# Performance work log

Hardware: AMD Instinct MI355X
Metric: run time of the kernel (lower is better)

## Reference

```python
import jax, jax.numpy as jnp
import numpy as np

B, H, W, C = 32, 56, 56, 192
NUM_HEADS = 6
WS = 7
SHIFT = 3
HIDDEN = 4 * C


def _relative_position_index(ws):
    coords = np.stack(np.meshgrid(np.arange(ws), np.arange(ws), indexing="ij"))  # 2,ws,ws
    coords = coords.reshape(2, -1)
    rel = coords[:, :, None] - coords[:, None, :]  # 2,N,N
    rel = rel.transpose(1, 2, 0)
    rel[:, :, 0] += ws - 1
    rel[:, :, 1] += ws - 1
    rel[:, :, 0] *= 2 * ws - 1
    return rel.sum(-1)  # N,N in [0, (2ws-1)^2)


def setup_inputs() -> dict:
    key = jax.random.key(0)
    ks = jax.random.split(key, 16)
    s = 0.02
    inp = {
        "x": jax.random.normal(ks[0], (B, H, W, C), jnp.float32),
        "norm1_g": jnp.ones((C,), jnp.float32),
        "norm1_b": jnp.zeros((C,), jnp.float32),
        "qkv_w": jax.random.normal(ks[1], (3 * C, C), jnp.float32) * s,
        "qkv_b": jnp.zeros((3 * C,), jnp.float32),
        "proj_w": jax.random.normal(ks[2], (C, C), jnp.float32) * s,
        "proj_b": jnp.zeros((C,), jnp.float32),
        "rel_bias_table": jax.random.normal(ks[3], ((2 * WS - 1) ** 2, NUM_HEADS), jnp.float32) * s,
        "norm2_g": jnp.ones((C,), jnp.float32),
        "norm2_b": jnp.zeros((C,), jnp.float32),
        "fc1_w": jax.random.normal(ks[4], (HIDDEN, C), jnp.float32) * s,
        "fc1_b": jnp.zeros((HIDDEN,), jnp.float32),
        "fc2_w": jax.random.normal(ks[5], (C, HIDDEN), jnp.float32) * s,
        "fc2_b": jnp.zeros((C,), jnp.float32),
        "rel_index": jnp.asarray(_relative_position_index(WS), jnp.int32),  # (49,49)
    }
    return inp


def _layernorm(x, g, b, eps=1e-5):
    mu = x.mean(-1, keepdims=True)
    var = ((x - mu) ** 2).mean(-1, keepdims=True)
    return (x - mu) * jax.lax.rsqrt(var + eps) * g + b


def _window_partition(x, ws):
    b, h, w, c = x.shape
    x = x.reshape(b, h // ws, ws, w // ws, ws, c)
    return x.transpose(0, 1, 3, 2, 4, 5).reshape(-1, ws * ws, c)


def _window_reverse(win, ws, b, h, w):
    c = win.shape[-1]
    x = win.reshape(b, h // ws, w // ws, ws, ws, c)
    return x.transpose(0, 1, 3, 2, 4, 5).reshape(b, h, w, c)


def reference(x, norm1_g, norm1_b, qkv_w, qkv_b, proj_w, proj_b, rel_bias_table,
              norm2_g, norm2_b, fc1_w, fc1_b, fc2_w, fc2_b, rel_index):
    shortcut = x
    xn = _layernorm(x, norm1_g, norm1_b)
    xs = jnp.roll(xn, (-SHIFT, -SHIFT), axis=(1, 2))
    win = _window_partition(xs, WS)  # (nW*B, 49, C)
    nw, n, c = win.shape
    hd = c // NUM_HEADS
    qkv = win @ qkv_w.T + qkv_b  # (nw, n, 3C)
    qkv = qkv.reshape(nw, n, 3, NUM_HEADS, hd).transpose(2, 0, 3, 1, 4)
    q, k, v = qkv[0], qkv[1], qkv[2]  # (nw, heads, n, hd)
    q = q * (hd ** -0.5)
    attn = jnp.einsum("whnd,whmd->whnm", q, k)
    bias = rel_bias_table[rel_index.reshape(-1)].reshape(n, n, NUM_HEADS).transpose(2, 0, 1)
    attn = jax.nn.softmax(attn + bias[None], axis=-1)
    out = jnp.einsum("whnm,whmd->whnd", attn, v)
    out = out.transpose(0, 2, 1, 3).reshape(nw, n, c)
    out = out @ proj_w.T + proj_b
    xs = _window_reverse(out, WS, x.shape[0], x.shape[1], x.shape[2])
    xa = jnp.roll(xs, (SHIFT, SHIFT), axis=(1, 2))
    x = shortcut + xa
    xm = _layernorm(x, norm2_g, norm2_b)
    xm = jax.nn.gelu(xm @ fc1_w.T + fc1_b, approximate=False)
    xm = xm @ fc2_w.T + fc2_b
    return x + xm
```

## Files before the change

### kernel.cpp

```cpp
#include <hip/hip_runtime.h>
#include <hip/hip_bf16.h>

#define CC 192
#define NHEADS 6
#define HDIM 32
#define NTOK 49
#define NWIN 2048
#define MTOK 100352
#define HIDDEN 768

typedef __hip_bfloat16 bf16;
typedef __attribute__((ext_vector_type(8))) short short8;
typedef __attribute__((ext_vector_type(4))) float f32x4;

__global__ __launch_bounds__(256) void k_wconv(
    const float* __restrict__ qw, const float* __restrict__ pw,
    const float* __restrict__ f1, const float* __restrict__ f2,
    bf16* __restrict__ o) {
  int i = blockIdx.x * 256 + threadIdx.x;
  if (i < 110592) o[i] = __float2bfloat16(qw[i]);
  else if (i < 147456) o[i] = __float2bfloat16(pw[i - 110592]);
  else if (i < 294912) o[i] = __float2bfloat16(f1[i - 147456]);
  else if (i < 442368) o[i] = __float2bfloat16(f2[i - 294912]);
}

__global__ __launch_bounds__(256) void k_bias(
    const float* __restrict__ table, const int* __restrict__ ridx,
    float* __restrict__ bias6) {
  int i = blockIdx.x * 256 + threadIdx.x;
  if (i >= 6 * 2401) return;
  int h = i / 2401, e = i - h * 2401;
  bias6[i] = table[ridx[e] * NHEADS + h];
}

template <int MODE, int NT, int KC, int MF>
__global__ __launch_bounds__(256) void k_gemm_areg(
    const void* __restrict__ Ap, const bf16* __restrict__ W,
    const float* __restrict__ bias, void* __restrict__ out0,
    const void* __restrict__ aux, const float* __restrict__ lng,
    const float* __restrict__ lnb) {
  constexpr int K = KC * 192;
  constexpr int N = NT * 64;
  __shared__ bf16 Bs[2][64 * 192];
  const int tid = threadIdx.x;
  const int wave = tid >> 6, lane = tid & 63;
  const int grp = lane >> 4, rA = lane & 15;
  const int cq = grp, cn = rA;
  const int m0 = blockIdx.x * (MF * 64);
  const int mrow = m0 + wave * (MF * 16);

  short8 areg[MF][KC * 6];
  if constexpr (MODE == 1) {
#pragma unroll
    for (int mt = 0; mt < MF; ++mt) {
      const bf16* arow =
          (const bf16*)Ap + (size_t)(mrow + mt * 16 + rA) * K + grp * 8;
#pragma unroll
      for (int kt = 0; kt < KC * 6; ++kt)
        areg[mt][kt] = *(const short8*)(arow + kt * 32);
    }
  } else {
#pragma unroll
    for (int mt = 0; mt < MF; ++mt) {
      int m = mrow + mt * 16 + rA;
      int w = m / 49, n = m - w * 49;
      int b = w >> 6, wrem = w & 63;
      int hi = wrem >> 3, wi = wrem & 7;
      int ii = n / 7, jj = n - ii * 7;
      int hs = hi * 7 + ii + 3; if (hs >= 56) hs -= 56;
      int wsc = wi * 7 + jj + 3; if (wsc >= 56) wsc -= 56;
      const float* rowp =
          (const float*)Ap + (size_t)((b * 56 + hs) * 56 + wsc) * CC;
      f32x4 xv[12];
#pragma unroll
      for (int kt = 0; kt < 6; ++kt) {
        xv[2 * kt]     = *(const f32x4*)(rowp + kt * 32 + grp * 8);
        xv[2 * kt + 1] = *(const f32x4*)(rowp + kt * 32 + grp * 8 + 4);
      }
      float s = 0.0f;
#pragma unroll
      for (int i = 0; i < 12; ++i)
#pragma unroll
        for (int j = 0; j < 4; ++j) s += xv[i][j];
      s += __shfl_xor(s, 16, 64);
      s += __shfl_xor(s, 32, 64);
      float mu = s * (1.0f / 192.0f);
      float q = 0.0f;
#pragma unroll
      for (int i = 0; i < 12; ++i)
#pragma unroll
        for (int j = 0; j < 4; ++j) {
          float d = xv[i][j] - mu;
          q += d * d;
        }
      q += __shfl_xor(q, 16, 64);
      q += __shfl_xor(q, 32, 64);
      float inv = rsqrtf(q * (1.0f / 192.0f) + 1e-5f);
#pragma unroll
      for (int kt = 0; kt < 6; ++kt) {
        short8 t;
#pragma unroll
        for (int j = 0; j < 8; ++j) {
          int col = kt * 32 + grp * 8 + j;
          float xval = xv[2 * kt + (j >> 2)][j & 3];
          float val = (xval - mu) * inv * lng[col] + lnb[col];
          bf16 hb = __float2bfloat16(val);
          t[j] = *reinterpret_cast<short*>(&hb);
        }
        areg[mt][kt] = t;
      }
    }
  }

  int rowoff[MF][4];
  if constexpr (MODE == 1) {
#pragma unroll
    for (int mt = 0; mt < MF; ++mt)
#pragma unroll
      for (int r = 0; r < 4; ++r) {
        int m = mrow + mt * 16 + cq * 4 + r;
        int w = m / 49, rr = m - w * 49;
        int b = w >> 6, wrem = w & 63;
        int hi = wrem >> 3, wi = wrem & 7;
        int ii = rr / 7, jj = rr - ii * 7;
        int hd = hi * 7 + ii + 3; if (hd >= 56) hd -= 56;
        int wd = wi * 7 + jj + 3; if (wd >= 56) wd -= 56;
        rowoff[mt][r] = ((b * 56 + hd) * 56 + wd) * CC;
      }
  }

  auto stage = [&](int buf, int nt, int kc) {
#pragma unroll
    for (int i = 0; i < 6; ++i) {
      int c = i * 256 + tid;
      int row = c / 24;
      int cbl = ((c - row * 24) * 16) ^ ((row & 7) << 4);
      const char* src = (const char*)W +
          (size_t)(nt * 64 + row) * (K * 2) + kc * 384 + cbl;
      __builtin_amdgcn_global_load_lds(
          (const __attribute__((address_space(1))) void*)src,
          (__attribute__((address_space(3))) void*)((char*)&Bs[buf][0] + c * 16),
          16, 0, 0);
    }
  };
  stage(0, 0, 0);

  f32x4 acc[MF][4];
#pragma unroll
  for (int s = 0; s < NT * KC; ++s) {
    const int nt = s / KC, kc = s - nt * KC;
    const int cur = s & 1;
    __syncthreads();
    if (s + 1 < NT * KC) stage(cur ^ 1, (s + 1) / KC, (s + 1) % KC);
    if (kc == 0) {
#pragma unroll
      for (int mt = 0; mt < MF; ++mt)
#pragma unroll
        for (int ntf = 0; ntf < 4; ++ntf)
          acc[mt][ntf] = (f32x4){0.f, 0.f, 0.f, 0.f};
    }
#pragma unroll
    for (int kt = 0; kt < 6; ++kt) {
      short8 b[4];
#pragma unroll
      for (int ntf = 0; ntf < 4; ++ntf) {
        int row = ntf * 16 + rA;
        int phys = row * 384 + ((kt * 64 + grp * 16) ^ ((row & 7) << 4));
        b[ntf] = *(const short8*)((const char*)&Bs[cur][0] + phys);
      }
#pragma unroll
      for (int mt = 0; mt < MF; ++mt)
#pragma unroll
        for (int ntf = 0; ntf < 4; ++ntf)
          acc[mt][ntf] = __builtin_amdgcn_mfma_f32_16x16x32_bf16(
              areg[mt][kc * 6 + kt], b[ntf], acc[mt][ntf], 0, 0, 0);
    }
    if (kc == KC - 1) {
      const int n0t = nt * 64;
      float bi[4];
#pragma unroll
      for (int ntf = 0; ntf < 4; ++ntf) bi[ntf] = bias[n0t + ntf * 16 + cn];
#pragma unroll
      for (int mt = 0; mt < MF; ++mt) {
#pragma unroll
        for (int r = 0; r < 4; ++r) {
          const int m = mrow + mt * 16 + cq * 4 + r;
#pragma unroll
          for (int ntf = 0; ntf < 4; ++ntf) {
            const int n = n0t + ntf * 16 + cn;
            float v = acc[mt][ntf][r] + bi[ntf];
            if constexpr (MODE == 0) {
              ((bf16*)out0)[(size_t)m * N + n] = __float2bfloat16(v);
            } else {
              float res = ((const float*)aux)[(size_t)rowoff[mt][r] + n];
              ((float*)out0)[(size_t)rowoff[mt][r] + n] = v + res;
            }
          }
        }
      }
    }
  }
}

__global__ __launch_bounds__(256) void k_mlp(
    const float* __restrict__ x1, const bf16* __restrict__ W1,
    const bf16* __restrict__ W2, const float* __restrict__ b1,
    const float* __restrict__ b2, float* __restrict__ out,
    const float* __restrict__ lng, const float* __restrict__ lnb) {
  __shared__ bf16 W1s[2][32 * 192];
  __shared__ bf16 W2s[2][192 * 32];
  __shared__ bf16 Hl[4][640];
  const int tid = threadIdx.x;
  const int wave = tid >> 6, lane = tid & 63;
  const int grp = lane >> 4, rA = lane & 15;
  const int mrow = blockIdx.x * 64 + wave * 16;
  char* hb = (char*)&Hl[wave][0];

  short8 areg[6];
  {
    const float* rowp = x1 + (size_t)(mrow + rA) * CC;
    f32x4 xv[12];
#pragma unroll
    for (int kt = 0; kt < 6; ++kt) {
      xv[2 * kt]     = *(const f32x4*)(rowp + kt * 32 + grp * 8);
      xv[2 * kt + 1] = *(const f32x4*)(rowp + kt * 32 + grp * 8 + 4);
    }
    float s = 0.0f;
#pragma unroll
    for (int i = 0; i < 12; ++i)
#pragma unroll
      for (int j = 0; j < 4; ++j) s += xv[i][j];
    s += __shfl_xor(s, 16, 64);
    s += __shfl_xor(s, 32, 64);
    float mu = s * (1.0f / 192.0f);
    float q = 0.0f;
#pragma unroll
    for (int i = 0; i < 12; ++i)
#pragma unroll
      for (int j = 0; j < 4; ++j) {
        float d = xv[i][j] - mu;
        q += d * d;
      }
    q += __shfl_xor(q, 16, 64);
    q += __shfl_xor(q, 32, 64);
    float inv = rsqrtf(q * (1.0f / 192.0f) + 1e-5f);
#pragma unroll
    for (int kt = 0; kt < 6; ++kt) {
      short8 t;
#pragma unroll
      for (int j = 0; j < 8; ++j) {
        int col = kt * 32 + grp * 8 + j;
        float xval = xv[2 * kt + (j >> 2)][j & 3];
        float val = (xval - mu) * inv * lng[col] + lnb[col];
        bf16 hbv = __float2bfloat16(val);
        t[j] = *reinterpret_cast<short*>(&hbv);
      }
      areg[kt] = t;
    }
  }

  auto stage1 = [&](int buf, int c) {
#pragma unroll
    for (int i = 0; i < 3; ++i) {
      int s = i * 256 + tid;
      int row = s / 24, slot = s - row * 24;
      int cbl = (slot * 16) ^ ((row & 7) << 4);
      const char* src = (const char*)W1 + (size_t)(c * 32 + row) * 384 + cbl;
      __builtin_amdgcn_global_load_lds(
          (const __attribute__((address_space(1))) void*)src,
          (__attribute__((address_space(3))) void*)((char*)&W1s[buf][0] + s * 16),
          16, 0, 0);
    }
  };
  auto stage2 = [&](int buf, int c) {
#pragma unroll
    for (int i = 0; i < 3; ++i) {
      int s = i * 256 + tid;
      int row = s >> 2, slot = s & 3;
      int cbl = (slot * 16) ^ (((row >> 1) & 3) << 4);
      const char* src = (const char*)W2 + (size_t)row * 1536 + c * 64 + cbl;
      __builtin_amdgcn_global_load_lds(
          (const __attribute__((address_space(1))) void*)src,
          (__attribute__((address_space(3))) void*)((char*)&W2s[buf][0] + s * 16),
          16, 0, 0);
    }
  };

  f32x4 acc2[12];
#pragma unroll
  for (int nf = 0; nf < 12; ++nf) acc2[nf] = (f32x4){0.f, 0.f, 0.f, 0.f};

  stage1(0, 0);
  stage2(0, 0);
  for (int c = 0; c < 24; ++c) {
    const int cur = c & 1;
    __syncthreads();
    if (c + 1 < 24) { stage1(cur ^ 1, c + 1); stage2(cur ^ 1, c + 1); }
    f32x4 fa[2] = {};
#pragma unroll
    for (int kt = 0; kt < 6; ++kt) {
      short8 bfr[2];
#pragma unroll
      for (int ntf = 0; ntf < 2; ++ntf) {
        int row = ntf * 16 + rA;
        int phys = row * 384 + ((kt * 64 + grp * 16) ^ ((row & 7) << 4));
        bfr[ntf] = *(const short8*)((const char*)&W1s[cur][0] + phys);
      }
#pragma unroll
      for (int ntf = 0; ntf < 2; ++ntf)
        fa[ntf] = __builtin_amdgcn_mfma_f32_16x16x32_bf16(
            areg[kt], bfr[ntf], fa[ntf], 0, 0, 0);
    }
#pragma unroll
    for (int ntf = 0; ntf < 2; ++ntf) {
      float b1v = b1[c * 32 + ntf * 16 + rA];
#pragma unroll
      for (int r = 0; r < 4; ++r) {
        float v = fa[ntf][r] + b1v;
        float u2 = 2.0f * v * (0.7978845608f + 0.0356774081f * v * v);
        float ge = v / (1.0f + __expf(-u2));
        int row = grp * 4 + r;
        *(bf16*)(hb + row * 80 + (ntf * 16 + rA) * 2) = __float2bfloat16(ge);
      }
    }
    short8 a2 = *(const short8*)(hb + rA * 80 + grp * 16);
#pragma unroll
    for (int nf = 0; nf < 12; ++nf) {
      int row = nf * 16 + rA;
      int phys = row * 64 + ((grp * 16) ^ (((row >> 1) & 3) << 4));
      short8 bw = *(const short8*)((const char*)&W2s[cur][0] + phys);
      acc2[nf] = __builtin_amdgcn_mfma_f32_16x16x32_bf16(a2, bw, acc2[nf],
                                                         0, 0, 0);
    }
  }

#pragma unroll
  for (int nf = 0; nf < 12; ++nf) {
    float b2v = b2[nf * 16 + rA];
#pragma unroll
    for (int r = 0; r < 4; ++r) {
      int m = mrow + grp * 4 + r;
      size_t idx = (size_t)m * CC + nf * 16 + rA;
      out[idx] = out[idx] + acc2[nf][r] + b2v;
    }
  }
}

__global__ __launch_bounds__(256) void k_attn_mfma(
    const bf16* __restrict__ qk, const float* __restrict__ bias6,
    bf16* __restrict__ ao) {
  __shared__ bf16 P[4][64 * 72];
  __shared__ bf16 VT[4][32 * 72];
  const int wave = threadIdx.x >> 6, lane = threadIdx.x & 63;
  const int wh = blockIdx.x * 4 + wave;
  const int w = wh / NHEADS, h = wh - w * NHEADS;
  const int rA = lane & 15, kq = (lane >> 4) * 8;
  const int grp = lane >> 4;

  const bf16* qbase = qk + (size_t)(w * 49) * 576 + h * HDIM + kq;

  short8 aq[4], bk[4], vrow[4];
#pragma unroll
  for (int t = 0; t < 4; ++t) {
    const bf16* rp = qbase + (size_t)(t * 16 + rA) * 576;
    aq[t] = *(const short8*)(rp);
    bk[t] = *(const short8*)(rp + 192);
    vrow[t] = *(const short8*)(rp + 384);
  }

  f32x4 S[4][4] = {};
#pragma unroll
  for (int mt = 0; mt < 4; ++mt)
#pragma unroll
    for (int nt = 0; nt < 4; ++nt)
      S[mt][nt] = __builtin_amdgcn_mfma_f32_16x16x32_bf16(
          aq[mt], bk[nt], S[mt][nt], 0, 0, 0);

  bf16* Vw = VT[wave];
  const bf16 zero = __float2bfloat16(0.0f);
#pragma unroll
  for (int t = 0; t < 4; ++t) {
    int tok = t * 16 + rA;
#pragma unroll
    for (int j = 0; j < 8; ++j)
      Vw[(kq + j) * 72 + tok] = (tok < 49) ? ((const bf16*)&vrow[t])[j] : zero;
  }

  const float scale = 0.17677669529663687f;
  const float* bh = bias6 + h * 2401;
  float rs[4][4];
  bf16* Pw = P[wave];
#pragma unroll
  for (int mt = 0; mt < 4; ++mt) {
#pragma unroll
    for (int r = 0; r < 4; ++r) {
      int row = mt * 16 + grp * 4 + r;
      float val[4];
#pragma unroll
      for (int nt = 0; nt < 4; ++nt) {
        int c = nt * 16 + rA;
        float bv = (row < 49 && c < 49) ? bh[row * 49 + c] : 0.0f;
        val[nt] = (c < 49) ? (S[mt][nt][r] * scale + bv) : -1e30f;
      }
      float mx = fmaxf(fmaxf(val[0], val[1]), fmaxf(val[2], val[3]));
      for (int m2 = 1; m2 < 16; m2 <<= 1) mx = fmaxf(mx, __shfl_xor(mx, m2, 64));
      float sum = 0.0f;
#pragma unroll
      for (int nt = 0; nt < 4; ++nt) {
        float e = __expf(val[nt] - mx);
        val[nt] = e;
        sum += e;
      }
      for (int m2 = 1; m2 < 16; m2 <<= 1) sum += __shfl_xor(sum, m2, 64);
      rs[mt][r] = 1.0f / sum;
#pragma unroll
      for (int nt = 0; nt < 4; ++nt)
        Pw[row * 72 + nt * 16 + rA] = __float2bfloat16(val[nt]);
    }
  }
  __syncthreads();

  short8 bv[2][2];
#pragma unroll
  for (int ks = 0; ks < 2; ++ks)
#pragma unroll
    for (int nt = 0; nt < 2; ++nt)
      bv[ks][nt] = *(const short8*)&Vw[(nt * 16 + rA) * 72 + ks * 32 + kq];
  f32x4 O[4][2] = {};
#pragma unroll
  for (int mt = 0; mt < 4; ++mt) {
    short8 ap0 = *(const short8*)&Pw[(mt * 16 + rA) * 72 + kq];
    short8 ap1 = *(const short8*)&Pw[(mt * 16 + rA) * 72 + 32 + kq];
#pragma unroll
    for (int nt = 0; nt < 2; ++nt) {
      O[mt][nt] = __builtin_amdgcn_mfma_f32_16x16x32_bf16(ap0, bv[0][nt],
                                                          O[mt][nt], 0, 0, 0);
      O[mt][nt] = __builtin_amdgcn_mfma_f32_16x16x32_bf16(ap1, bv[1][nt],
                                                          O[mt][nt], 0, 0, 0);
    }
  }
#pragma unroll
  for (int mt = 0; mt < 4; ++mt) {
#pragma unroll
    for (int r = 0; r < 4; ++r) {
      int m = mt * 16 + grp * 4 + r;
      if (m < 49) {
        bf16* orow = ao + (size_t)(w * 49 + m) * CC + h * HDIM;
#pragma unroll
        for (int nt = 0; nt < 2; ++nt)
          orow[nt * 16 + rA] = __float2bfloat16(O[mt][nt][r] * rs[mt][r]);
      }
    }
  }
}

extern "C" void kernel_launch(void* const* d_in, const int* in_sizes, int n_in,
                              void* d_out, int out_size, void* d_ws, size_t ws_size,
                              hipStream_t stream) {
  const float* x        = (const float*)d_in[0];
  const float* norm1_g  = (const float*)d_in[1];
  const float* norm1_b  = (const float*)d_in[2];
  const float* qkv_w    = (const float*)d_in[3];
  const float* qkv_b    = (const float*)d_in[4];
  const float* proj_w   = (const float*)d_in[5];
  const float* proj_b   = (const float*)d_in[6];
  const float* rel_tab  = (const float*)d_in[7];
  const float* norm2_g  = (const float*)d_in[8];
  const float* norm2_b  = (const float*)d_in[9];
  const float* fc1_w    = (const float*)d_in[10];
  const float* fc1_b    = (const float*)d_in[11];
  const float* fc2_w    = (const float*)d_in[12];
  const float* fc2_b    = (const float*)d_in[13];
  const int*   rel_idx  = (const int*)d_in[14];
  float* out = (float*)d_out;

  char* ws = (char*)d_ws;
  bf16*  qkb   = (bf16*)ws;
  bf16*  ao    = (bf16*)(ws + 115605504);
  bf16*  wbuf  = (bf16*)(ws + 154140672);
  float* bias6 = (float*)(ws + 155025408);
  float* x1    = out;
  bf16* wq = wbuf;
  bf16* wp = wbuf + 110592;
  bf16* w1 = wbuf + 147456;
  bf16* w2 = wbuf + 294912;

  k_wconv<<<1728, 256, 0, stream>>>(qkv_w, proj_w, fc1_w, fc2_w, wbuf);
  k_bias<<<57, 256, 0, stream>>>(rel_tab, rel_idx, bias6);
  k_gemm_areg<0, 9, 1, 1><<<MTOK / 64, 256, 0, stream>>>(
      x, wq, qkv_b, qkb, nullptr, norm1_g, norm1_b);
  k_attn_mfma<<<NWIN * NHEADS / 4, 256, 0, stream>>>(qkb, bias6, ao);
  k_gemm_areg<1, 3, 1, 2><<<MTOK / 128, 256, 0, stream>>>(
      ao, wp, proj_b, x1, x, nullptr, nullptr);
  k_mlp<<<MTOK / 64, 256, 0, stream>>>(
      x1, w1, w2, fc1_b, fc2_b, out, norm2_g, norm2_b);
}
```

Before: 463.4 us.

## Use 512-thread blocks for GEMM and MLP kernels; split weight staging across halves

Result: slower. 498.7 us (+7.6%).

```diff
diff --git a/kernel.cpp b/kernel.cpp
--- a/kernel.cpp
+++ b/kernel.cpp
@@ -33,20 +33,22 @@
   bias6[i] = table[ridx[e] * NHEADS + h];
 }
 
-template <int MODE, int NT, int KC, int MF>
-__global__ __launch_bounds__(256) void k_gemm_areg(
+template <int MODE, int NT, int KC, int MF, int TPB>
+__global__ __launch_bounds__(TPB) void k_gemm_areg(
     const void* __restrict__ Ap, const bf16* __restrict__ W,
     const float* __restrict__ bias, void* __restrict__ out0,
     const void* __restrict__ aux, const float* __restrict__ lng,
     const float* __restrict__ lnb) {
   constexpr int K = KC * 192;
   constexpr int N = NT * 64;
+  constexpr int BROWS = (TPB / 64) * MF * 16;
+  constexpr int SLOT_IT = 1536 / TPB;
   __shared__ bf16 Bs[2][64 * 192];
   const int tid = threadIdx.x;
   const int wave = tid >> 6, lane = tid & 63;
   const int grp = lane >> 4, rA = lane & 15;
   const int cq = grp, cn = rA;
-  const int m0 = blockIdx.x * (MF * 64);
+  const int m0 = blockIdx.x * BROWS;
   const int mrow = m0 + wave * (MF * 16);
 
   short8 areg[MF][KC * 6];
@@ -131,8 +133,8 @@
 
   auto stage = [&](int buf, int nt, int kc) {
 #pragma unroll
-    for (int i = 0; i < 6; ++i) {
-      int c = i * 256 + tid;
+    for (int i = 0; i < SLOT_IT; ++i) {
+      int c = i * TPB + tid;
       int row = c / 24;
       int cbl = ((c - row * 24) * 16) ^ ((row & 7) << 4);
       const char* src = (const char*)W +
@@ -202,18 +204,18 @@
   }
 }
 
-__global__ __launch_bounds__(256) void k_mlp(
+__global__ __launch_bounds__(512) void k_mlp(
     const float* __restrict__ x1, const bf16* __restrict__ W1,
     const bf16* __restrict__ W2, const float* __restrict__ b1,
     const float* __restrict__ b2, float* __restrict__ out,
     const float* __restrict__ lng, const float* __restrict__ lnb) {
   __shared__ bf16 W1s[2][32 * 192];
   __shared__ bf16 W2s[2][192 * 32];
-  __shared__ bf16 Hl[4][640];
+  __shared__ bf16 Hl[8][640];
   const int tid = threadIdx.x;
   const int wave = tid >> 6, lane = tid & 63;
   const int grp = lane >> 4, rA = lane & 15;
-  const int mrow = blockIdx.x * 64 + wave * 16;
+  const int mrow = blockIdx.x * 128 + wave * 16;
   char* hb = (char*)&Hl[wave][0];
 
   short8 areg[6];
@@ -259,43 +261,40 @@
     }
   }
 
-  auto stage1 = [&](int buf, int c) {
+  auto stageW = [&](int buf, int c) {
+    int t2 = tid & 255;
 #pragma unroll
     for (int i = 0; i < 3; ++i) {
-      int s = i * 256 + tid;
-      int row = s / 24, slot = s - row * 24;
-      int cbl = (slot * 16) ^ ((row & 7) << 4);
-      const char* src = (const char*)W1 + (size_t)(c * 32 + row) * 384 + cbl;
-      __builtin_amdgcn_global_load_lds(
-          (const __attribute__((address_space(1))) void*)src,
-          (__attribute__((address_space(3))) void*)((char*)&W1s[buf][0] + s * 16),
-          16, 0, 0);
+      int s = i * 256 + t2;
+      if (tid < 256) {
+        int row = s / 24, slot = s - row * 24;
+        int cbl = (slot * 16) ^ ((row & 7) << 4);
+        const char* src = (const char*)W1 + (size_t)(c * 32 + row) * 384 + cbl;
+        __builtin_amdgcn_global_load_lds(
+            (const __attribute__((address_space(1))) void*)src,
+            (__attribute__((address_space(3))) void*)((char*)&W1s[buf][0] + s * 16),
+            16, 0, 0);
+      } else {
+        int row = s >> 2, slot = s & 3;
+        int cbl = (slot * 16) ^ (((row >> 1) & 3) << 4);
+        const char* src = (const char*)W2 + (size_t)row * 1536 + c * 64 + cbl;
+        __builtin_amdgcn_global_load_lds(
+            (const __attribute__((address_space(1))) void*)src,
+            (__attribute__((address_space(3))) void*)((char*)&W2s[buf][0] + s * 16),
+            16, 0, 0);
+      }
     }
   };
-  auto stage2 = [&](int buf, int c) {
-#pragma unroll
-    for (int i = 0; i < 3; ++i) {
-      int s = i * 256 + tid;
-      int row = s >> 2, slot = s & 3;
-      int cbl = (slot * 16) ^ (((row >> 1) & 3) << 4);
-      const char* src = (const char*)W2 + (size_t)row * 1536 + c * 64 + cbl;
-      __builtin_amdgcn_global_load_lds(
-          (const __attribute__((address_space(1))) void*)src,
-          (__attribute__((address_space(3))) void*)((char*)&W2s[buf][0] + s * 16),
-          16, 0, 0);
-    }
-  };
 
   f32x4 acc2[12];
 #pragma unroll
   for (int nf = 0; nf < 12; ++nf) acc2[nf] = (f32x4){0.f, 0.f, 0.f, 0.f};
 
-  stage1(0, 0);
-  stage2(0, 0);
+  stageW(0, 0);
   for (int c = 0; c < 24; ++c) {
     const int cur = c & 1;
     __syncthreads();
-    if (c + 1 < 24) { stage1(cur ^ 1, c + 1); stage2(cur ^ 1, c + 1); }
+    if (c + 1 < 24) stageW(cur ^ 1, c + 1);
     f32x4 fa[2] = {};
 #pragma unroll
     for (int kt = 0; kt < 6; ++kt) {
@@ -418,7 +417,6 @@
         Pw[row * 72 + nt * 16 + rA] = __float2bfloat16(val[nt]);
     }
   }
-  __syncthreads();
 
   short8 bv[2][2];
 #pragma unroll
@@ -487,11 +485,11 @@
 
   k_wconv<<<1728, 256, 0, stream>>>(qkv_w, proj_w, fc1_w, fc2_w, wbuf);
   k_bias<<<57, 256, 0, stream>>>(rel_tab, rel_idx, bias6);
-  k_gemm_areg<0, 9, 1, 1><<<MTOK / 64, 256, 0, stream>>>(
+  k_gemm_areg<0, 9, 1, 1, 512><<<MTOK / 128, 512, 0, stream>>>(
       x, wq, qkv_b, qkb, nullptr, norm1_g, norm1_b);
   k_attn_mfma<<<NWIN * NHEADS / 4, 256, 0, stream>>>(qkb, bias6, ao);
-  k_gemm_areg<1, 3, 1, 2><<<MTOK / 128, 256, 0, stream>>>(
+  k_gemm_areg<1, 3, 1, 1, 512><<<MTOK / 128, 512, 0, stream>>>(
       ao, wp, proj_b, x1, x, nullptr, nullptr);
-  k_mlp<<<MTOK / 64, 256, 0, stream>>>(
+  k_mlp<<<MTOK / 128, 512, 0, stream>>>(
       x1, w1, w2, fc1_b, fc2_b, out, norm2_g, norm2_b);
 }
```

## Double MLP rows per wave to reuse staged fc1/fc2 weight fragments

Applied to the files above, without the earlier changes.

New measurement: 566.9 us. 22.3% more time.

```diff
diff --git a/kernel.cpp b/kernel.cpp
--- a/kernel.cpp
+++ b/kernel.cpp
@@ -11,6 +11,7 @@
 
 typedef __hip_bfloat16 bf16;
 typedef __attribute__((ext_vector_type(8))) short short8;
+typedef __attribute__((ext_vector_type(4))) short short4v;
 typedef __attribute__((ext_vector_type(4))) float f32x4;
 
 __global__ __launch_bounds__(256) void k_wconv(
@@ -46,7 +47,7 @@
   const int wave = tid >> 6, lane = tid & 63;
   const int grp = lane >> 4, rA = lane & 15;
   const int cq = grp, cn = rA;
-  const int m0 = blockIdx.x * (MF * 64);
+  const int m0 = blockIdx.x * (4 * MF * 16);
   const int mrow = m0 + wave * (MF * 16);
 
   short8 areg[MF][KC * 6];
@@ -209,16 +210,17 @@
     const float* __restrict__ lng, const float* __restrict__ lnb) {
   __shared__ bf16 W1s[2][32 * 192];
   __shared__ bf16 W2s[2][192 * 32];
-  __shared__ bf16 Hl[4][640];
+  __shared__ bf16 Hl[4][32 * 40];
   const int tid = threadIdx.x;
   const int wave = tid >> 6, lane = tid & 63;
   const int grp = lane >> 4, rA = lane & 15;
-  const int mrow = blockIdx.x * 64 + wave * 16;
+  const int mrow = blockIdx.x * 128 + wave * 32;
   char* hb = (char*)&Hl[wave][0];
 
-  short8 areg[6];
-  {
-    const float* rowp = x1 + (size_t)(mrow + rA) * CC;
+  short8 areg[2][6];
+#pragma unroll
+  for (int mt = 0; mt < 2; ++mt) {
+    const float* rowp = x1 + (size_t)(mrow + mt * 16 + rA) * CC;
     f32x4 xv[12];
 #pragma unroll
     for (int kt = 0; kt < 6; ++kt) {
@@ -255,7 +257,7 @@
         bf16 hbv = __float2bfloat16(val);
         t[j] = *reinterpret_cast<short*>(&hbv);
       }
-      areg[kt] = t;
+      areg[mt][kt] = t;
     }
   }
 
@@ -286,9 +288,11 @@
     }
   };
 
-  f32x4 acc2[12];
-#pragma unroll
-  for (int nf = 0; nf < 12; ++nf) acc2[nf] = (f32x4){0.f, 0.f, 0.f, 0.f};
+  f32x4 acc2[2][12];
+#pragma unroll
+  for (int mt = 0; mt < 2; ++mt)
+#pragma unroll
+    for (int nf = 0; nf < 12; ++nf) acc2[mt][nf] = (f32x4){0.f, 0.f, 0.f, 0.f};
 
   stage1(0, 0);
   stage2(0, 0);
@@ -296,41 +300,47 @@
     const int cur = c & 1;
     __syncthreads();
     if (c + 1 < 24) { stage1(cur ^ 1, c + 1); stage2(cur ^ 1, c + 1); }
-    f32x4 fa[2] = {};
-#pragma unroll
-    for (int kt = 0; kt < 6; ++kt) {
-      short8 bfr[2];
-#pragma unroll
-      for (int ntf = 0; ntf < 2; ++ntf) {
-        int row = ntf * 16 + rA;
+#pragma unroll
+    for (int s = 0; s < 2; ++s) {
+      f32x4 fa[2] = {};
+#pragma unroll
+      for (int kt = 0; kt < 6; ++kt) {
+        int row = s * 16 + rA;
         int phys = row * 384 + ((kt * 64 + grp * 16) ^ ((row & 7) << 4));
-        bfr[ntf] = *(const short8*)((const char*)&W1s[cur][0] + phys);
-      }
-#pragma unroll
-      for (int ntf = 0; ntf < 2; ++ntf)
-        fa[ntf] = __builtin_amdgcn_mfma_f32_16x16x32_bf16(
-            areg[kt], bfr[ntf], fa[ntf], 0, 0, 0);
-    }
-#pragma unroll
-    for (int ntf = 0; ntf < 2; ++ntf) {
-      float b1v = b1[c * 32 + ntf * 16 + rA];
-#pragma unroll
-      for (int r = 0; r < 4; ++r) {
-        float v = fa[ntf][r] + b1v;
-        float u2 = 2.0f * v * (0.7978845608f + 0.0356774081f * v * v);
-        float ge = v / (1.0f + __expf(-u2));
-        int row = grp * 4 + r;
-        *(bf16*)(hb + row * 80 + (ntf * 16 + rA) * 2) = __float2bfloat16(ge);
-      }
-    }
-    short8 a2 = *(const short8*)(hb + rA * 80 + grp * 16);
+        short8 wfr = *(const short8*)((const char*)&W1s[cur][0] + phys);
+#pragma unroll
+        for (int mt = 0; mt < 2; ++mt)
+          fa[mt] = __builtin_amdgcn_mfma_f32_16x16x32_bf16(
+              wfr, areg[mt][kt], fa[mt], 0, 0, 0);
+      }
+      f32x4 b1v = *(const f32x4*)(b1 + c * 32 + s * 16 + grp * 4);
+#pragma unroll
+      for (int mt = 0; mt < 2; ++mt) {
+        short4v hv;
+#pragma unroll
+        for (int r = 0; r < 4; ++r) {
+          float v = fa[mt][r] + b1v[r];
+          float u2 = 2.0f * v * (0.7978845608f + 0.0356774081f * v * v);
+          float ge = v / (1.0f + __expf(-u2));
+          bf16 gb = __float2bfloat16(ge);
+          hv[r] = *reinterpret_cast<short*>(&gb);
+        }
+        *(short4v*)(hb + (mt * 16 + rA) * 80 + s * 32 + grp * 8) = hv;
+      }
+    }
+    short8 a2[2];
+#pragma unroll
+    for (int mt = 0; mt < 2; ++mt)
+      a2[mt] = *(const short8*)(hb + (mt * 16 + rA) * 80 + grp * 16);
 #pragma unroll
     for (int nf = 0; nf < 12; ++nf) {
       int row = nf * 16 + rA;
       int phys = row * 64 + ((grp * 16) ^ (((row >> 1) & 3) << 4));
       short8 bw = *(const short8*)((const char*)&W2s[cur][0] + phys);
-      acc2[nf] = __builtin_amdgcn_mfma_f32_16x16x32_bf16(a2, bw, acc2[nf],
-                                                         0, 0, 0);
+#pragma unroll
+      for (int mt = 0; mt < 2; ++mt)
+        acc2[mt][nf] = __builtin_amdgcn_mfma_f32_16x16x32_bf16(
+            a2[mt], bw, acc2[mt][nf], 0, 0, 0);
     }
   }
 
@@ -338,10 +348,13 @@
   for (int nf = 0; nf < 12; ++nf) {
     float b2v = b2[nf * 16 + rA];
 #pragma unroll
-    for (int r = 0; r < 4; ++r) {
-      int m = mrow + grp * 4 + r;
-      size_t idx = (size_t)m * CC + nf * 16 + rA;
-      out[idx] = out[idx] + acc2[nf][r] + b2v;
+    for (int mt = 0; mt < 2; ++mt) {
+#pragma unroll
+      for (int r = 0; r < 4; ++r) {
+        int m = mrow + mt * 16 + grp * 4 + r;
+        size_t idx = (size_t)m * CC + nf * 16 + rA;
+        out[idx] = out[idx] + acc2[mt][nf][r] + b2v;
+      }
     }
   }
 }
@@ -492,6 +505,6 @@
   k_attn_mfma<<<NWIN * NHEADS / 4, 256, 0, stream>>>(qkb, bias6, ao);
   k_gemm_areg<1, 3, 1, 2><<<MTOK / 128, 256, 0, stream>>>(
       ao, wp, proj_b, x1, x, nullptr, nullptr);
-  k_mlp<<<MTOK / 64, 256, 0, stream>>>(
+  k_mlp<<<MTOK / 128, 256, 0, stream>>>(
       x1, w1, w2, fc1_b, fc2_b, out, norm2_g, norm2_b);
 }
```
